# Kernel tuning notes

Hardware: AMD Instinct MI355X
Metric: run time of the kernel (lower is better)

Reference implementation:

```python
import jax, jax.numpy as jnp
import numpy as np

N_NODES = 100000

def _graphconv(x, edge_src, edge_dst, norm_src, norm_dst, W, b):
    # DGL GraphConv with norm='both': D_out^{-1/2} A D_in^{-1/2} X W + b
    h = x * norm_src[:, None]                       # [N, d] src normalization
    msg = jnp.take(h, edge_src, axis=0)             # [E, d] gather
    agg = jax.ops.segment_sum(msg, edge_dst, num_segments=N_NODES)  # [N, d] scatter-add
    h = agg * norm_dst[:, None]                      # dst normalization
    return h @ W + b

def _degree_norms(edge_src, edge_dst):
    ones = jnp.ones(edge_src.shape[0], dtype=jnp.float32)
    deg_out = jax.ops.segment_sum(ones, edge_src, num_segments=N_NODES)
    deg_in = jax.ops.segment_sum(ones, edge_dst, num_segments=N_NODES)
    norm_src = jnp.where(deg_out > 0, jax.lax.rsqrt(jnp.maximum(deg_out, 1.0)), 0.0)
    norm_dst = jnp.where(deg_in > 0, jax.lax.rsqrt(jnp.maximum(deg_in, 1.0)), 0.0)
    return norm_src, norm_dst

def setup_inputs() -> dict:
    key = jax.random.key(0)
    ks = jax.random.split(key, 8)
    E = 1600000
    in_f, h_f, out_f = 128, 128, 64
    x = jax.random.normal(ks[0], (N_NODES, in_f), dtype=jnp.float32)
    edge_src = jax.random.randint(ks[1], (E,), 0, N_NODES, dtype=jnp.int32)
    edge_dst = jax.random.randint(ks[2], (E,), 0, N_NODES, dtype=jnp.int32)
    def glorot(k, shape):
        lim = np.sqrt(6.0 / (shape[0] + shape[1]))
        return jax.random.uniform(k, shape, jnp.float32, -lim, lim)
    W0 = glorot(ks[3], (in_f, h_f)); b0 = jnp.zeros((h_f,), jnp.float32)
    W1 = glorot(ks[4], (h_f, h_f)); b1 = jnp.zeros((h_f,), jnp.float32)
    W2 = glorot(ks[5], (h_f, out_f)); b2 = jnp.zeros((out_f,), jnp.float32)
    return {"x": x, "edge_src": edge_src, "edge_dst": edge_dst,
            "W0": W0, "b0": b0, "W1": W1, "b1": b1, "W2": W2, "b2": b2}

def reference(x, edge_src, edge_dst, W0, b0, W1, b1, W2, b2):
    norm_src, norm_dst = _degree_norms(edge_src, edge_dst)
    outputs = [x]
    h = jax.nn.relu(_graphconv(x, edge_src, edge_dst, norm_src, norm_dst, W0, b0))
    outputs.append(h)
    h = jax.nn.relu(_graphconv(h, edge_src, edge_dst, norm_src, norm_dst, W1, b1))
    outputs.append(h)
    h = _graphconv(h, edge_src, edge_dst, norm_src, norm_dst, W2, b2)
    outputs.append(h)
    return tuple(outputs)
```

## Files before the change

kernel.cpp:

```cpp
#include <hip/hip_runtime.h>

#define NN 100000
#define NE 1600000
#define NB 391
#define RS 32768
#define KR 4
#define RSL 64
#define SLICE 25000

typedef unsigned int uint;
typedef unsigned short ushort;
typedef unsigned char uchar;
typedef __attribute__((ext_vector_type(8))) short short8;
typedef __attribute__((ext_vector_type(4))) float f32x4;

__device__ __forceinline__ ushort f2bf(float f) {
    uint u = __float_as_uint(f);
    return (ushort)((u + 0x7FFFu + ((u >> 16) & 1u)) >> 16);
}

__device__ __forceinline__ void bf8_add(uint4 q, float* acc) {
    acc[0] += __uint_as_float(q.x << 16);
    acc[1] += __uint_as_float(q.x & 0xFFFF0000u);
    acc[2] += __uint_as_float(q.y << 16);
    acc[3] += __uint_as_float(q.y & 0xFFFF0000u);
    acc[4] += __uint_as_float(q.z << 16);
    acc[5] += __uint_as_float(q.z & 0xFFFF0000u);
    acc[6] += __uint_as_float(q.w << 16);
    acc[7] += __uint_as_float(q.w & 0xFFFF0000u);
}


__global__ __launch_bounds__(256)
void k_hist(const int* __restrict__ src, const int* __restrict__ dst,
            uchar* __restrict__ pout, uchar* __restrict__ pin) {
    int k = blockIdx.x >> 6, r = blockIdx.x & 63;
    __shared__ uint ho[RS / 4], hi[RS / 4];
    for (int i = threadIdx.x; i < RS / 4; i += 256) { ho[i] = 0; hi[i] = 0; }
    __syncthreads();
    int base = k * RS;
    int lo = r * SLICE, hiend = lo + SLICE;
    for (int i = lo + threadIdx.x; i < hiend; i += 256) {
        int s = src[i] - base;
        if ((uint)s < RS) atomicAdd(&ho[s >> 2], 1u << (8 * (s & 3)));
        int d = dst[i] - base;
        if ((uint)d < RS) atomicAdd(&hi[d >> 2], 1u << (8 * (d & 3)));
    }
    __syncthreads();
    uint* po = (uint*)(pout + ((size_t)k * RSL + r) * RS);
    uint* pi = (uint*)(pin + ((size_t)k * RSL + r) * RS);
    for (int i = threadIdx.x; i < RS / 4; i += 256) { po[i] = ho[i]; pi[i] = hi[i]; }
}


__global__ void k_red(const uchar* __restrict__ pout, uchar* __restrict__ pin,
                      float* __restrict__ ns, float* __restrict__ nd,
                      int* __restrict__ csum) {
    int n = blockIdx.x * 256 + threadIdx.x;
    if (n >= NN) return;
    int k = n >> 15, j = n & (RS - 1);
    const uchar* po = pout + (size_t)k * RSL * RS + j;
    uchar* pi = pin + (size_t)k * RSL * RS + j;
    int so = 0;
    #pragma unroll
    for (int r = 0; r < RSL; ++r) so += po[(size_t)r * RS];
    int si = 0;
    #pragma unroll
    for (int r = 0; r < RSL; ++r) {
        uchar c = pi[(size_t)r * RS];
        pi[(size_t)r * RS] = (uchar)si;
        si += c;
    }
    ns[n] = (so > 0) ? rsqrtf((float)so) : 0.f;
    nd[n] = (si > 0) ? rsqrtf((float)si) : 0.f;
    csum[n] = si;
}


__global__ void k_blocksum(const int* __restrict__ cnt, int* __restrict__ bsum) {
    __shared__ int s[256];
    int t = threadIdx.x;
    int i = blockIdx.x * 256 + t;
    s[t] = (i < NN) ? cnt[i] : 0;
    __syncthreads();
    for (int off = 128; off > 0; off >>= 1) {
        if (t < off) s[t] += s[t + off];
        __syncthreads();
    }
    if (t == 0) bsum[blockIdx.x] = s[0];
}

__global__ void k_scanb(const int* __restrict__ bsum, int* __restrict__ bsumex,
                        int* __restrict__ rowptr) {
    __shared__ int s[512];
    int t = threadIdx.x;
    int v = (t < NB) ? bsum[t] : 0;
    s[t] = v;
    __syncthreads();
    for (int off = 1; off < 512; off <<= 1) {
        int add = (t >= off) ? s[t - off] : 0;
        __syncthreads();
        s[t] += add;
        __syncthreads();
    }
    if (t < NB) bsumex[t] = s[t] - v;
    if (t == 0) rowptr[NN] = NE;
}

__global__ void k_rowptr(const int* __restrict__ cnt, const int* __restrict__ bsumex,
                         int* __restrict__ rowptr) {
    __shared__ int s[256];
    int t = threadIdx.x;
    int i = blockIdx.x * 256 + t;
    int v = (i < NN) ? cnt[i] : 0;
    s[t] = v;
    __syncthreads();
    for (int off = 1; off < 256; off <<= 1) {
        int add = (t >= off) ? s[t - off] : 0;
        __syncthreads();
        s[t] += add;
        __syncthreads();
    }
    if (i < NN) rowptr[i] = bsumex[blockIdx.x] + s[t] - v;
}


__global__ __launch_bounds__(256)
void k_fill(const int* __restrict__ src, const int* __restrict__ dst,
            const uchar* __restrict__ pin, const int* __restrict__ rowptr,
            int* __restrict__ csrc) {
    int k = blockIdx.x >> 6, r = blockIdx.x & 63;
    __shared__ uint cur[RS / 2];
    const uchar* pi = pin + ((size_t)k * RSL + r) * RS;
    for (int i = threadIdx.x; i < RS / 2; i += 256) {
        uint a = pi[2 * i], b = pi[2 * i + 1];
        cur[i] = a | (b << 16);
    }
    __syncthreads();
    int base = k * RS;
    int lo = r * SLICE, hiend = lo + SLICE;
    for (int i = lo + threadIdx.x; i < hiend; i += 256) {
        int d = dst[i];
        int j = d - base;
        if ((uint)j < RS) {
            uint old = atomicAdd(&cur[j >> 1], 1u << (16 * (j & 1)));
            int p = (old >> (16 * (j & 1))) & 0xFFFF;
            csrc[rowptr[d] + p] = src[i];
        }
    }
}


template<int N>
__global__ void k_wt(const float* __restrict__ W, ushort* __restrict__ WT) {
    int i = blockIdx.x * 256 + threadIdx.x;
    if (i < N * 128) {
        int n = i >> 7, k = i & 127;
        WT[i] = f2bf(W[k * N + n]);
    }
}


template<int NT, int N, bool COPY>
__global__ __launch_bounds__(256)
void k_gemm_mfma(const float* __restrict__ A, const ushort* __restrict__ WT,
                 const float* __restrict__ ns, ushort* __restrict__ Cb,
                 float* __restrict__ xout) {
    int tid = threadIdx.x;
    int w = tid >> 6;
    int l = tid & 63;
    int li = l & 15;
    int kg = l >> 4;
    short8 bfrag[NT][4];
    #pragma unroll
    for (int n = 0; n < NT; ++n) {
        int col = w * 16 * NT + n * 16 + li;
        #pragma unroll
        for (int kt = 0; kt < 4; ++kt)
            bfrag[n][kt] = *(const short8*)(WT + (size_t)col * 128 + kt * 32 + kg * 8);
    }
    for (int mg = blockIdx.x; mg < NN / 16; mg += gridDim.x) {
        int row = mg * 16 + li;
        short8 afrag[4];
        #pragma unroll
        for (int kt = 0; kt < 4; ++kt) {
            const float* ap = A + (size_t)row * 128 + kt * 32 + kg * 8;
            float4 a0 = *(const float4*)ap;
            float4 a1 = *(const float4*)(ap + 4);
            if (COPY && w == 0) {
                float* op = xout + (size_t)row * 128 + kt * 32 + kg * 8;
                *(float4*)op = a0;
                *(float4*)(op + 4) = a1;
            }
            short8 af;
            af[0] = (short)f2bf(a0.x); af[1] = (short)f2bf(a0.y);
            af[2] = (short)f2bf(a0.z); af[3] = (short)f2bf(a0.w);
            af[4] = (short)f2bf(a1.x); af[5] = (short)f2bf(a1.y);
            af[6] = (short)f2bf(a1.z); af[7] = (short)f2bf(a1.w);
            afrag[kt] = af;
        }
        int crow = mg * 16 + kg * 4;
        float4 nsv = *(const float4*)(ns + crow);
        float nsa[4] = {nsv.x, nsv.y, nsv.z, nsv.w};
        #pragma unroll
        for (int n = 0; n < NT; ++n) {
            f32x4 acc = {0.f, 0.f, 0.f, 0.f};
            #pragma unroll
            for (int kt = 0; kt < 4; ++kt)
                acc = __builtin_amdgcn_mfma_f32_16x16x32_bf16(afrag[kt], bfrag[n][kt], acc, 0, 0, 0);
            int ccol = w * 16 * NT + n * 16 + li;
            #pragma unroll
            for (int r = 0; r < 4; ++r)
                Cb[(size_t)(crow + r) * N + ccol] = f2bf(acc[r] * nsa[r]);
        }
    }
}


template<bool RELU>
__global__ __launch_bounds__(256)
void k_agg128(const ushort* __restrict__ Yb, const int* __restrict__ rowptr,
              const int* __restrict__ csrc, const float* __restrict__ nd,
              const float* __restrict__ bias, float* __restrict__ out) {
    int tid = threadIdx.x;
    int grp = tid >> 4;
    int lane = tid & 15;
    int node = blockIdx.x * 16 + grp;
    int beg = rowptr[node], end = rowptr[node + 1];
    float acc[8] = {0.f, 0.f, 0.f, 0.f, 0.f, 0.f, 0.f, 0.f};
    int e = beg;
    for (; e + 3 < end; e += 4) {
        int s0 = csrc[e];     int s1 = csrc[e + 1];
        int s2 = csrc[e + 2]; int s3 = csrc[e + 3];
        uint4 q0 = *(const uint4*)(Yb + (size_t)s0 * 128 + lane * 8);
        uint4 q1 = *(const uint4*)(Yb + (size_t)s1 * 128 + lane * 8);
        uint4 q2 = *(const uint4*)(Yb + (size_t)s2 * 128 + lane * 8);
        uint4 q3 = *(const uint4*)(Yb + (size_t)s3 * 128 + lane * 8);
        bf8_add(q0, acc); bf8_add(q1, acc); bf8_add(q2, acc); bf8_add(q3, acc);
    }
    for (; e < end; ++e) {
        uint4 q = *(const uint4*)(Yb + (size_t)csrc[e] * 128 + lane * 8);
        bf8_add(q, acc);
    }
    float ndv = nd[node];
    float4 b0 = *(const float4*)(bias + lane * 8);
    float4 b1 = *(const float4*)(bias + lane * 8 + 4);
    float4 o0, o1;
    o0.x = acc[0] * ndv + b0.x; o0.y = acc[1] * ndv + b0.y;
    o0.z = acc[2] * ndv + b0.z; o0.w = acc[3] * ndv + b0.w;
    o1.x = acc[4] * ndv + b1.x; o1.y = acc[5] * ndv + b1.y;
    o1.z = acc[6] * ndv + b1.z; o1.w = acc[7] * ndv + b1.w;
    if (RELU) {
        o0.x = fmaxf(o0.x, 0.f); o0.y = fmaxf(o0.y, 0.f);
        o0.z = fmaxf(o0.z, 0.f); o0.w = fmaxf(o0.w, 0.f);
        o1.x = fmaxf(o1.x, 0.f); o1.y = fmaxf(o1.y, 0.f);
        o1.z = fmaxf(o1.z, 0.f); o1.w = fmaxf(o1.w, 0.f);
    }
    *(float4*)(out + (size_t)node * 128 + lane * 8)     = o0;
    *(float4*)(out + (size_t)node * 128 + lane * 8 + 4) = o1;
}

__global__ __launch_bounds__(256)
void k_agg64(const ushort* __restrict__ Yb, const int* __restrict__ rowptr,
             const int* __restrict__ csrc, const float* __restrict__ nd,
             const float* __restrict__ bias, float* __restrict__ out) {
    int tid = threadIdx.x;
    int grp = tid >> 3;
    int lane = tid & 7;
    int node = blockIdx.x * 32 + grp;
    int beg = rowptr[node], end = rowptr[node + 1];
    float acc[8] = {0.f, 0.f, 0.f, 0.f, 0.f, 0.f, 0.f, 0.f};
    int e = beg;
    for (; e + 3 < end; e += 4) {
        int s0 = csrc[e];     int s1 = csrc[e + 1];
        int s2 = csrc[e + 2]; int s3 = csrc[e + 3];
        uint4 q0 = *(const uint4*)(Yb + (size_t)s0 * 64 + lane * 8);
        uint4 q1 = *(const uint4*)(Yb + (size_t)s1 * 64 + lane * 8);
        uint4 q2 = *(const uint4*)(Yb + (size_t)s2 * 64 + lane * 8);
        uint4 q3 = *(const uint4*)(Yb + (size_t)s3 * 64 + lane * 8);
        bf8_add(q0, acc); bf8_add(q1, acc); bf8_add(q2, acc); bf8_add(q3, acc);
    }
    for (; e < end; ++e) {
        uint4 q = *(const uint4*)(Yb + (size_t)csrc[e] * 64 + lane * 8);
        bf8_add(q, acc);
    }
    float ndv = nd[node];
    float4 b0 = *(const float4*)(bias + lane * 8);
    float4 b1 = *(const float4*)(bias + lane * 8 + 4);
    float4 o0, o1;
    o0.x = acc[0] * ndv + b0.x; o0.y = acc[1] * ndv + b0.y;
    o0.z = acc[2] * ndv + b0.z; o0.w = acc[3] * ndv + b0.w;
    o1.x = acc[4] * ndv + b1.x; o1.y = acc[5] * ndv + b1.y;
    o1.z = acc[6] * ndv + b1.z; o1.w = acc[7] * ndv + b1.w;
    *(float4*)(out + (size_t)node * 64 + lane * 8)     = o0;
    *(float4*)(out + (size_t)node * 64 + lane * 8 + 4) = o1;
}


extern "C" void kernel_launch(void* const* d_in, const int* in_sizes, int n_in,
                              void* d_out, int out_size, void* d_ws, size_t ws_size,
                              hipStream_t stream) {
    const float* x  = (const float*)d_in[0];
    const int* esrc = (const int*)d_in[1];
    const int* edst = (const int*)d_in[2];
    const float* W0 = (const float*)d_in[3];
    const float* b0 = (const float*)d_in[4];
    const float* W1 = (const float*)d_in[5];
    const float* b1 = (const float*)d_in[6];
    const float* W2 = (const float*)d_in[7];
    const float* b2 = (const float*)d_in[8];
    float* out = (float*)d_out;

    float* ns      = (float*)d_ws;
    float* nd      = ns + NN;
    int*   csum    = (int*)(nd + NN);
    int*   rowptr  = csum + NN;
    int*   bsum    = rowptr + NN + 8;
    int*   bsumex  = bsum + 512;
    int*   csrc    = bsumex + 512;
    uchar* pout    = (uchar*)(csrc + NE);
    uchar* pin     = pout + (size_t)KR * RSL * RS;
    ushort* WT0    = (ushort*)(pin + (size_t)KR * RSL * RS);
    ushort* WT1    = WT0 + 128 * 128;
    ushort* WT2    = WT1 + 128 * 128;
    ushort* Y2b    = WT2 + 64 * 128;

    float* h1 = out + (size_t)NN * 128;
    float* h2 = h1 + (size_t)NN * 128;
    float* h3 = h2 + (size_t)NN * 128;

    ushort* Y0b = (ushort*)h2;
    ushort* Y1b = (ushort*)h3;

    k_hist<<<KR * RSL, 256, 0, stream>>>(esrc, edst, pout, pin);

    k_red<<<(NN + 255) / 256, 256, 0, stream>>>(pout, pin, ns, nd, csum);

    k_blocksum<<<NB, 256, 0, stream>>>(csum, bsum);
    k_scanb<<<1, 512, 0, stream>>>(bsum, bsumex, rowptr);
    k_rowptr<<<NB, 256, 0, stream>>>(csum, bsumex, rowptr);

    k_fill<<<KR * RSL, 256, 0, stream>>>(esrc, edst, pin, rowptr, csrc);

    k_wt<128><<<64, 256, 0, stream>>>(W0, WT0);
    k_wt<128><<<64, 256, 0, stream>>>(W1, WT1);
    k_wt<64><<<32, 256, 0, stream>>>(W2, WT2);

    k_gemm_mfma<2, 128, true><<<1024, 256, 0, stream>>>(x, WT0, ns, Y0b, out);
    k_agg128<true><<<NN / 16, 256, 0, stream>>>(Y0b, rowptr, csrc, nd, b0, h1);

    k_gemm_mfma<2, 128, false><<<1024, 256, 0, stream>>>(h1, WT1, ns, Y1b, nullptr);
    k_agg128<true><<<NN / 16, 256, 0, stream>>>(Y1b, rowptr, csrc, nd, b1, h2);

    k_gemm_mfma<1, 64, false><<<1024, 256, 0, stream>>>(h2, WT2, ns, Y2b, nullptr);
    k_agg64<<<NN / 32, 256, 0, stream>>>(Y2b, rowptr, csrc, nd, b2, h3);
}
```

Baseline: 439.9 us.

## Fuse block sums into reduce, batch weight casts, emit bf16 activations, unroll gathers

Folds the per-block degree sum into the k_red kernel and merges the three weight-transpose launches into one, cutting launch count. The aggregation kernels now also write a bf16 copy of their output. A separate conversion kernel produces bf16 x, so the GEMMs read half-width activations instead of converting fp32 on the fly. The gather loops are unrolled to 8 edges for more memory-level parallelism. In exchange, the aggregation kernels write extra bf16 buffers and there is an additional x-conversion pass.

```diff
diff --git a/kernel.cpp b/kernel.cpp
--- a/kernel.cpp
+++ b/kernel.cpp
@@ -53,42 +53,40 @@
 }
 
 
-__global__ void k_red(const uchar* __restrict__ pout, uchar* __restrict__ pin,
-                      float* __restrict__ ns, float* __restrict__ nd,
-                      int* __restrict__ csum) {
-    int n = blockIdx.x * 256 + threadIdx.x;
-    if (n >= NN) return;
-    int k = n >> 15, j = n & (RS - 1);
-    const uchar* po = pout + (size_t)k * RSL * RS + j;
-    uchar* pi = pin + (size_t)k * RSL * RS + j;
-    int so = 0;
-    #pragma unroll
-    for (int r = 0; r < RSL; ++r) so += po[(size_t)r * RS];
+__global__ __launch_bounds__(256)
+void k_red(const uchar* __restrict__ pout, uchar* __restrict__ pin,
+           float* __restrict__ ns, float* __restrict__ nd,
+           int* __restrict__ csum, int* __restrict__ bsum) {
+    __shared__ int sred[256];
+    int t = threadIdx.x;
+    int n = blockIdx.x * 256 + t;
     int si = 0;
-    #pragma unroll
-    for (int r = 0; r < RSL; ++r) {
-        uchar c = pi[(size_t)r * RS];
-        pi[(size_t)r * RS] = (uchar)si;
-        si += c;
-    }
-    ns[n] = (so > 0) ? rsqrtf((float)so) : 0.f;
-    nd[n] = (si > 0) ? rsqrtf((float)si) : 0.f;
-    csum[n] = si;
-}
-
-
-__global__ void k_blocksum(const int* __restrict__ cnt, int* __restrict__ bsum) {
-    __shared__ int s[256];
-    int t = threadIdx.x;
-    int i = blockIdx.x * 256 + t;
-    s[t] = (i < NN) ? cnt[i] : 0;
+    if (n < NN) {
+        int k = n >> 15, j = n & (RS - 1);
+        const uchar* po = pout + (size_t)k * RSL * RS + j;
+        uchar* pi = pin + (size_t)k * RSL * RS + j;
+        int so = 0;
+        #pragma unroll
+        for (int r = 0; r < RSL; ++r) so += po[(size_t)r * RS];
+        #pragma unroll
+        for (int r = 0; r < RSL; ++r) {
+            uchar c = pi[(size_t)r * RS];
+            pi[(size_t)r * RS] = (uchar)si;
+            si += c;
+        }
+        ns[n] = (so > 0) ? rsqrtf((float)so) : 0.f;
+        nd[n] = (si > 0) ? rsqrtf((float)si) : 0.f;
+        csum[n] = si;
+    }
+    sred[t] = si;
     __syncthreads();
     for (int off = 128; off > 0; off >>= 1) {
-        if (t < off) s[t] += s[t + off];
-        __syncthreads();
-    }
-    if (t == 0) bsum[blockIdx.x] = s[0];
-}
+        if (t < off) sred[t] += sred[t + off];
+        __syncthreads();
+    }
+    if (t == 0) bsum[blockIdx.x] = sred[0];
+}
+
 
 __global__ void k_scanb(const int* __restrict__ bsum, int* __restrict__ bsumex,
                         int* __restrict__ rowptr) {
@@ -151,21 +149,39 @@
 }
 
 
-template<int N>
-__global__ void k_wt(const float* __restrict__ W, ushort* __restrict__ WT) {
+__global__ void k_wtall(const float* __restrict__ W0, const float* __restrict__ W1,
+                        const float* __restrict__ W2, ushort* __restrict__ WT) {
     int i = blockIdx.x * 256 + threadIdx.x;
-    if (i < N * 128) {
+    if (i < 16384) {
         int n = i >> 7, k = i & 127;
-        WT[i] = f2bf(W[k * N + n]);
-    }
-}
-
-
-template<int NT, int N, bool COPY>
-__global__ __launch_bounds__(256)
-void k_gemm_mfma(const float* __restrict__ A, const ushort* __restrict__ WT,
-                 const float* __restrict__ ns, ushort* __restrict__ Cb,
-                 float* __restrict__ xout) {
+        WT[i] = f2bf(W0[k * 128 + n]);
+    } else if (i < 32768) {
+        int j = i - 16384; int n = j >> 7, k = j & 127;
+        WT[i] = f2bf(W1[k * 128 + n]);
+    } else if (i < 40960) {
+        int j = i - 32768; int n = j >> 7, k = j & 127;
+        WT[i] = f2bf(W2[k * 64 + n]);
+    }
+}
+
+
+__global__ void k_xcvt(const float4* __restrict__ x, float4* __restrict__ out,
+                       ushort* __restrict__ xb, int n4) {
+    int i = blockIdx.x * blockDim.x + threadIdx.x;
+    if (i < n4) {
+        float4 v = x[i];
+        out[i] = v;
+        ushort4 b;
+        b.x = f2bf(v.x); b.y = f2bf(v.y); b.z = f2bf(v.z); b.w = f2bf(v.w);
+        *(ushort4*)(xb + (size_t)i * 4) = b;
+    }
+}
+
+
+template<int NT, int N>
+__global__ __launch_bounds__(256)
+void k_gemm_mfma(const ushort* __restrict__ Ab, const ushort* __restrict__ WT,
+                 const float* __restrict__ ns, ushort* __restrict__ Cb) {
     int tid = threadIdx.x;
     int w = tid >> 6;
     int l = tid & 63;
@@ -183,22 +199,8 @@
         int row = mg * 16 + li;
         short8 afrag[4];
         #pragma unroll
-        for (int kt = 0; kt < 4; ++kt) {
-            const float* ap = A + (size_t)row * 128 + kt * 32 + kg * 8;
-            float4 a0 = *(const float4*)ap;
-            float4 a1 = *(const float4*)(ap + 4);
-            if (COPY && w == 0) {
-                float* op = xout + (size_t)row * 128 + kt * 32 + kg * 8;
-                *(float4*)op = a0;
-                *(float4*)(op + 4) = a1;
-            }
-            short8 af;
-            af[0] = (short)f2bf(a0.x); af[1] = (short)f2bf(a0.y);
-            af[2] = (short)f2bf(a0.z); af[3] = (short)f2bf(a0.w);
-            af[4] = (short)f2bf(a1.x); af[5] = (short)f2bf(a1.y);
-            af[6] = (short)f2bf(a1.z); af[7] = (short)f2bf(a1.w);
-            afrag[kt] = af;
-        }
+        for (int kt = 0; kt < 4; ++kt)
+            afrag[kt] = *(const short8*)(Ab + (size_t)row * 128 + kt * 32 + kg * 8);
         int crow = mg * 16 + kg * 4;
         float4 nsv = *(const float4*)(ns + crow);
         float nsa[4] = {nsv.x, nsv.y, nsv.z, nsv.w};
@@ -221,7 +223,8 @@
 __global__ __launch_bounds__(256)
 void k_agg128(const ushort* __restrict__ Yb, const int* __restrict__ rowptr,
               const int* __restrict__ csrc, const float* __restrict__ nd,
-              const float* __restrict__ bias, float* __restrict__ out) {
+              const float* __restrict__ bias, float* __restrict__ out,
+              ushort* __restrict__ outb) {
     int tid = threadIdx.x;
     int grp = tid >> 4;
     int lane = tid & 15;
@@ -229,6 +232,22 @@
     int beg = rowptr[node], end = rowptr[node + 1];
     float acc[8] = {0.f, 0.f, 0.f, 0.f, 0.f, 0.f, 0.f, 0.f};
     int e = beg;
+    for (; e + 7 < end; e += 8) {
+        int s0 = csrc[e];     int s1 = csrc[e + 1];
+        int s2 = csrc[e + 2]; int s3 = csrc[e + 3];
+        int s4 = csrc[e + 4]; int s5 = csrc[e + 5];
+        int s6 = csrc[e + 6]; int s7 = csrc[e + 7];
+        uint4 q0 = *(const uint4*)(Yb + (size_t)s0 * 128 + lane * 8);
+        uint4 q1 = *(const uint4*)(Yb + (size_t)s1 * 128 + lane * 8);
+        uint4 q2 = *(const uint4*)(Yb + (size_t)s2 * 128 + lane * 8);
+        uint4 q3 = *(const uint4*)(Yb + (size_t)s3 * 128 + lane * 8);
+        uint4 q4 = *(const uint4*)(Yb + (size_t)s4 * 128 + lane * 8);
+        uint4 q5 = *(const uint4*)(Yb + (size_t)s5 * 128 + lane * 8);
+        uint4 q6 = *(const uint4*)(Yb + (size_t)s6 * 128 + lane * 8);
+        uint4 q7 = *(const uint4*)(Yb + (size_t)s7 * 128 + lane * 8);
+        bf8_add(q0, acc); bf8_add(q1, acc); bf8_add(q2, acc); bf8_add(q3, acc);
+        bf8_add(q4, acc); bf8_add(q5, acc); bf8_add(q6, acc); bf8_add(q7, acc);
+    }
     for (; e + 3 < end; e += 4) {
         int s0 = csrc[e];     int s1 = csrc[e + 1];
         int s2 = csrc[e + 2]; int s3 = csrc[e + 3];
@@ -245,19 +264,21 @@
     float ndv = nd[node];
     float4 b0 = *(const float4*)(bias + lane * 8);
     float4 b1 = *(const float4*)(bias + lane * 8 + 4);
-    float4 o0, o1;
-    o0.x = acc[0] * ndv + b0.x; o0.y = acc[1] * ndv + b0.y;
-    o0.z = acc[2] * ndv + b0.z; o0.w = acc[3] * ndv + b0.w;
-    o1.x = acc[4] * ndv + b1.x; o1.y = acc[5] * ndv + b1.y;
-    o1.z = acc[6] * ndv + b1.z; o1.w = acc[7] * ndv + b1.w;
+    float o[8];
+    o[0] = acc[0] * ndv + b0.x; o[1] = acc[1] * ndv + b0.y;
+    o[2] = acc[2] * ndv + b0.z; o[3] = acc[3] * ndv + b0.w;
+    o[4] = acc[4] * ndv + b1.x; o[5] = acc[5] * ndv + b1.y;
+    o[6] = acc[6] * ndv + b1.z; o[7] = acc[7] * ndv + b1.w;
     if (RELU) {
-        o0.x = fmaxf(o0.x, 0.f); o0.y = fmaxf(o0.y, 0.f);
-        o0.z = fmaxf(o0.z, 0.f); o0.w = fmaxf(o0.w, 0.f);
-        o1.x = fmaxf(o1.x, 0.f); o1.y = fmaxf(o1.y, 0.f);
-        o1.z = fmaxf(o1.z, 0.f); o1.w = fmaxf(o1.w, 0.f);
-    }
-    *(float4*)(out + (size_t)node * 128 + lane * 8)     = o0;
-    *(float4*)(out + (size_t)node * 128 + lane * 8 + 4) = o1;
+        #pragma unroll
+        for (int i = 0; i < 8; ++i) o[i] = fmaxf(o[i], 0.f);
+    }
+    *(float4*)(out + (size_t)node * 128 + lane * 8)     = make_float4(o[0], o[1], o[2], o[3]);
+    *(float4*)(out + (size_t)node * 128 + lane * 8 + 4) = make_float4(o[4], o[5], o[6], o[7]);
+    short8 ob;
+    #pragma unroll
+    for (int i = 0; i < 8; ++i) ob[i] = (short)f2bf(o[i]);
+    *(short8*)(outb + (size_t)node * 128 + lane * 8) = ob;
 }
 
 __global__ __launch_bounds__(256)
@@ -271,6 +292,22 @@
     int beg = rowptr[node], end = rowptr[node + 1];
     float acc[8] = {0.f, 0.f, 0.f, 0.f, 0.f, 0.f, 0.f, 0.f};
     int e = beg;
+    for (; e + 7 < end; e += 8) {
+        int s0 = csrc[e];     int s1 = csrc[e + 1];
+        int s2 = csrc[e + 2]; int s3 = csrc[e + 3];
+        int s4 = csrc[e + 4]; int s5 = csrc[e + 5];
+        int s6 = csrc[e + 6]; int s7 = csrc[e + 7];
+        uint4 q0 = *(const uint4*)(Yb + (size_t)s0 * 64 + lane * 8);
+        uint4 q1 = *(const uint4*)(Yb + (size_t)s1 * 64 + lane * 8);
+        uint4 q2 = *(const uint4*)(Yb + (size_t)s2 * 64 + lane * 8);
+        uint4 q3 = *(const uint4*)(Yb + (size_t)s3 * 64 + lane * 8);
+        uint4 q4 = *(const uint4*)(Yb + (size_t)s4 * 64 + lane * 8);
+        uint4 q5 = *(const uint4*)(Yb + (size_t)s5 * 64 + lane * 8);
+        uint4 q6 = *(const uint4*)(Yb + (size_t)s6 * 64 + lane * 8);
+        uint4 q7 = *(const uint4*)(Yb + (size_t)s7 * 64 + lane * 8);
+        bf8_add(q0, acc); bf8_add(q1, acc); bf8_add(q2, acc); bf8_add(q3, acc);
+        bf8_add(q4, acc); bf8_add(q5, acc); bf8_add(q6, acc); bf8_add(q7, acc);
+    }
     for (; e + 3 < end; e += 4) {
         int s0 = csrc[e];     int s1 = csrc[e + 1];
         int s2 = csrc[e + 2]; int s3 = csrc[e + 3];
@@ -324,6 +361,9 @@
     ushort* WT1    = WT0 + 128 * 128;
     ushort* WT2    = WT1 + 128 * 128;
     ushort* Y2b    = WT2 + 64 * 128;
+    ushort* xb     = Y2b + (size_t)NN * 64;
+    ushort* h1b    = xb + (size_t)NN * 128;
+    ushort* h2b    = h1b + (size_t)NN * 128;
 
     float* h1 = out + (size_t)NN * 128;
     float* h2 = h1 + (size_t)NN * 128;
@@ -334,24 +374,24 @@
 
     k_hist<<<KR * RSL, 256, 0, stream>>>(esrc, edst, pout, pin);
 
-    k_red<<<(NN + 255) / 256, 256, 0, stream>>>(pout, pin, ns, nd, csum);
-
-    k_blocksum<<<NB, 256, 0, stream>>>(csum, bsum);
+    k_red<<<NB, 256, 0, stream>>>(pout, pin, ns, nd, csum, bsum);
+
     k_scanb<<<1, 512, 0, stream>>>(bsum, bsumex, rowptr);
     k_rowptr<<<NB, 256, 0, stream>>>(csum, bsumex, rowptr);
 
     k_fill<<<KR * RSL, 256, 0, stream>>>(esrc, edst, pin, rowptr, csrc);
 
-    k_wt<128><<<64, 256, 0, stream>>>(W0, WT0);
-    k_wt<128><<<64, 256, 0, stream>>>(W1, WT1);
-    k_wt<64><<<32, 256, 0, stream>>>(W2, WT2);
-
-    k_gemm_mfma<2, 128, true><<<1024, 256, 0, stream>>>(x, WT0, ns, Y0b, out);
-    k_agg128<true><<<NN / 16, 256, 0, stream>>>(Y0b, rowptr, csrc, nd, b0, h1);
-
-    k_gemm_mfma<2, 128, false><<<1024, 256, 0, stream>>>(h1, WT1, ns, Y1b, nullptr);
-    k_agg128<true><<<NN / 16, 256, 0, stream>>>(Y1b, rowptr, csrc, nd, b1, h2);
-
-    k_gemm_mfma<1, 64, false><<<1024, 256, 0, stream>>>(h2, WT2, ns, Y2b, nullptr);
+    k_wtall<<<160, 256, 0, stream>>>(W0, W1, W2, WT0);
+
+    k_xcvt<<<(NN * 32 + 255) / 256, 256, 0, stream>>>((const float4*)x, (float4*)out,
+                                                      xb, NN * 32);
+
+    k_gemm_mfma<2, 128><<<1024, 256, 0, stream>>>(xb, WT0, ns, Y0b);
+    k_agg128<true><<<NN / 16, 256, 0, stream>>>(Y0b, rowptr, csrc, nd, b0, h1, h1b);
+
+    k_gemm_mfma<2, 128><<<1024, 256, 0, stream>>>(h1b, WT1, ns, Y1b);
+    k_agg128<true><<<NN / 16, 256, 0, stream>>>(Y1b, rowptr, csrc, nd, b1, h2, h2b);
+
+    k_gemm_mfma<1, 64><<<1024, 256, 0, stream>>>(h2b, WT2, ns, Y2b);
     k_agg64<<<NN / 32, 256, 0, stream>>>(Y2b, rowptr, csrc, nd, b2, h3);
 }
```

New measurement: 436.4 us. Within noise of the previous version (-0.8%).
